# Optimization experiments

Measured on AMD Instinct MI355X. Metric: run time of the kernel, lower is better.

## Reference

```python
import jax, jax.numpy as jnp
import numpy as np

EPS = 1e-5


def conv1x1(x, w):
    # x: (N, C, V, T), w: (O, C) -> (N, O, V, T)
    return jnp.einsum('ncvt,oc->novt', x, w)


def batchnorm2d(y, gamma, beta):
    # training-mode BN over (N, V, T) per channel, biased variance (torch semantics)
    mean = jnp.mean(y, axis=(0, 2, 3), keepdims=True)
    var = jnp.mean((y - mean) ** 2, axis=(0, 2, 3), keepdims=True)
    yhat = (y - mean) * jax.lax.rsqrt(var + EPS)
    return yhat * gamma[None, :, None, None] + beta[None, :, None, None]


def spatial_g(x, wg1, wg2):
    # learned adjacency: softmax over last dim of (N, T, V, V)
    a1 = conv1x1(x, wg1)  # (N, O, V, T)
    a2 = conv1x1(x, wg2)  # (N, O, V, T)
    g = jnp.einsum('novt,nout->ntvu', a1, a2)  # (N, T, V, V)
    return jax.nn.softmax(g, axis=-1)


def gcn_unit(x, g, w1, w2, gamma, beta):
    # message passing: g (N,T,V,V) applied over joint dim of x (N,C,V,T)
    x1 = jnp.einsum('ntvu,ncut->ncvt', g, x)
    y = conv1x1(x1, w1) + conv1x1(x, w2)
    return jax.nn.relu(batchnorm2d(y, gamma, beta))


def setup_inputs() -> dict:
    key = jax.random.key(0)
    ks = jax.random.split(key, 12)
    N, C, V, T = 64, 64, 25, 128
    dims = [64, 64, 128, 256]
    gp = 16
    s = 0.05
    inp = {
        'x': jax.random.normal(ks[0], (N, C, V, T), jnp.float32),
        'wg1': jax.random.normal(ks[1], (gp, dims[0]), jnp.float32) * s,
        'wg2': jax.random.normal(ks[2], (gp, dims[0]), jnp.float32) * s,
        'w11': jax.random.normal(ks[3], (dims[1], dims[0]), jnp.float32) * s,
        'w12': jax.random.normal(ks[4], (dims[1], dims[0]), jnp.float32) * s,
        'gamma1': jnp.ones((dims[1],), jnp.float32),
        'beta1': jnp.zeros((dims[1],), jnp.float32),
        'w21': jax.random.normal(ks[5], (dims[2], dims[1]), jnp.float32) * s,
        'w22': jax.random.normal(ks[6], (dims[2], dims[1]), jnp.float32) * s,
        'gamma2': jnp.ones((dims[2],), jnp.float32),
        'beta2': jnp.zeros((dims[2],), jnp.float32),
        'w31': jax.random.normal(ks[7], (dims[3], dims[2]), jnp.float32) * s,
        'w32': jax.random.normal(ks[8], (dims[3], dims[2]), jnp.float32) * s,
        'gamma3': jnp.ones((dims[3],), jnp.float32),
        'beta3': jnp.zeros((dims[3],), jnp.float32),
    }
    return inp


def reference(x, wg1, wg2, w11, w12, gamma1, beta1, w21, w22, gamma2, beta2,
              w31, w32, gamma3, beta3):
    g = spatial_g(x, wg1, wg2)                       # shared adjacency (N,T,V,V)
    x = gcn_unit(x, g, w11, w12, gamma1, beta1)      # (N, 64, V, T)
    x = gcn_unit(x, g, w21, w22, gamma2, beta2)      # (N, 128, V, T)
    x = gcn_unit(x, g, w31, w32, gamma3, beta3)      # (N, 256, V, T)
    return x, g
```

## Files before the change

kernel.cpp:

```cpp
#include <hip/hip_runtime.h>
#include <cstdint>

#define V_ 25
#define T_ 128
#define VT_ 3200
#define NVTF_ 204800.0f

typedef unsigned short ushort_t;
typedef __attribute__((ext_vector_type(8))) short s16x8;
typedef __attribute__((ext_vector_type(4))) float f32x4;

__device__ __forceinline__ ushort_t f2bf(float f) {
    union { float f; unsigned u; } v; v.f = f;
    unsigned r = v.u + 0x7FFFu + ((v.u >> 16) & 1u);
    return (ushort_t)(r >> 16);
}
__device__ __forceinline__ float bf2f(ushort_t h) {
    union { unsigned u; float f; } v; v.u = ((unsigned)h) << 16;
    return v.f;
}
__device__ __forceinline__ void gload16(const void* g, void* l) {
    __builtin_amdgcn_global_load_lds((const __attribute__((address_space(1))) void*)g,
                                     (__attribute__((address_space(3))) void*)l, 16, 0, 0);
}

__global__ __launch_bounds__(128) void k_a(const float* __restrict__ x,
        const float* __restrict__ wg1, const float* __restrict__ wg2,
        ushort_t* __restrict__ a1, ushort_t* __restrict__ a2,
        ushort_t* __restrict__ xb) {
    int b = blockIdx.x; int n = b / V_; int v = b % V_;
    int t = threadIdx.x;
    __shared__ float w1s[1024], w2s[1024];
    for (int i = threadIdx.x; i < 1024; i += 128) { w1s[i] = wg1[i]; w2s[i] = wg2[i]; }
    __syncthreads();
    float s1[16], s2[16];
    #pragma unroll
    for (int o = 0; o < 16; o++) { s1[o] = 0.f; s2[o] = 0.f; }
    s16x8 xs[8];
    const float* xp = x + (size_t)n * 204800 + v * T_ + t;
    #pragma unroll
    for (int c = 0; c < 64; c++) {
        float xv = xp[(size_t)c * VT_];
        xs[c >> 3][c & 7] = (short)f2bf(xv);
        #pragma unroll
        for (int o = 0; o < 16; o++) {
            s1[o] = fmaf(w1s[o*64+c], xv, s1[o]);
            s2[o] = fmaf(w2s[o*64+c], xv, s2[o]);
        }
    }
    size_t abase = (size_t)n * 51200 + v * T_ + t;
    #pragma unroll
    for (int o = 0; o < 16; o++) {
        a1[abase + (size_t)o * VT_] = f2bf(s1[o]);
        a2[abase + (size_t)o * VT_] = f2bf(s2[o]);
    }
    ushort_t* cp = xb + (size_t)(n * VT_ + v * T_ + t) * 64;
    #pragma unroll
    for (int ch = 0; ch < 8; ch++) *(s16x8*)(cp + ch * 8) = xs[ch];
}

__global__ __launch_bounds__(256) void k_g(const ushort_t* __restrict__ a1,
        const ushort_t* __restrict__ a2, float* __restrict__ g,
        ushort_t* __restrict__ gb) {
    int n = blockIdx.x >> 3; int t0 = (blockIdx.x & 7) * 16;
    __shared__ float A1s[6400], A2s[6400];
    for (int i = threadIdx.x; i < 6400; i += 256) {
        int o = i / 400; int r = i % 400; int v = r >> 4; int tt = r & 15;
        size_t ga = (size_t)n * 51200 + (size_t)o * VT_ + v * T_ + t0 + tt;
        A1s[i] = bf2f(a1[ga]);
        A2s[i] = bf2f(a2[ga]);
    }
    __syncthreads();
    for (int r = threadIdx.x; r < 400; r += 256) {
        int v = r >> 4; int tt = r & 15;
        float a1r[16];
        #pragma unroll
        for (int o = 0; o < 16; o++) a1r[o] = A1s[o*400 + v*16 + tt];
        float gr[25];
        float mx = -1e30f;
        for (int u = 0; u < 25; u++) {
            float s = 0.f;
            #pragma unroll
            for (int o = 0; o < 16; o++) s = fmaf(a1r[o], A2s[o*400 + u*16 + tt], s);
            gr[u] = s; mx = fmaxf(mx, s);
        }
        float sum = 0.f;
        for (int u = 0; u < 25; u++) { gr[u] = __expf(gr[u] - mx); sum += gr[u]; }
        float inv = 1.f / sum;
        float* gp = g + ((size_t)(n * T_ + t0 + tt) * V_ + v) * V_;
        ushort_t* gbp = gb + ((size_t)((n * 128 + t0 + tt) * 25 + v)) * 32;
        for (int u = 0; u < 25; u++) {
            float val = gr[u] * inv;
            gp[u] = val;
            gbp[u] = f2bf(val);
        }
    }
}

__global__ void k_wcat(const float* __restrict__ w11, const float* __restrict__ w12,
        const float* __restrict__ w21, const float* __restrict__ w22,
        const float* __restrict__ w31, const float* __restrict__ w32,
        ushort_t* __restrict__ Wc) {
    int i = blockIdx.x * 256 + threadIdx.x;
    float v;
    if (i < 8192) {
        int o = i >> 7, k = i & 127;
        v = (k < 64) ? w11[o * 64 + k] : w12[o * 64 + k - 64];
    } else if (i < 24576) {
        int j = i - 8192; int o = j >> 7, k = j & 127;
        v = (k < 64) ? w21[o * 64 + k] : w22[o * 64 + k - 64];
    } else {
        int j = i - 24576; int o = j >> 8, k = j & 255;
        v = (k < 128) ? w31[o * 128 + k] : w32[o * 128 + k - 128];
    }
    Wc[i] = f2bf(v);
}

template<int C, bool BNB, bool XBSRC, int TOUT, int OPASS>
__global__ __launch_bounds__(256) void k_fgemm(
        const ushort_t* __restrict__ Wc, const ushort_t* __restrict__ ysrc,
        const ushort_t* __restrict__ gb,
        const float* __restrict__ bns, const float* __restrict__ bnb,
        ushort_t* __restrict__ yt,
        float* __restrict__ psum, float* __restrict__ psq) {
    constexpr int K2 = 2 * C;
    constexpr int KSTEPS = K2 / 32;
    constexpr int NC8 = C / 8;
    constexpr int HKS = C / 32;
    constexpr int MROWS = 100;
    constexpr int MI = 7;
    constexpr int CW = (C == 64) ? 1 : 2;
    constexpr int XBYTES = (TOUT == 0) ? 14400 : 11200;
    __shared__ __align__(16) ushort_t YS[MROWS * C];
    __shared__ __align__(16) ushort_t MPo[MROWS * C];
    __shared__ __align__(16) char XTRA[XBYTES];
    float* GS = (float*)XTRA;
    ushort_t* Lw = (ushort_t*)XTRA;

    int n = blockIdx.y, mb = blockIdx.x;
    int m0 = mb * MROWS, tb = mb * 4;
    int tid = threadIdx.x, w = tid >> 6, lane = tid & 63;
    int l15 = lane & 15, g4 = lane >> 4;

    for (int i = tid; i < 2500; i += 256) {
        int tl = i / 625, r = i % 625, u = r / 25, v = r % 25;
        GS[(tl * 25 + u) * 28 + v] =
            bf2f(gb[((size_t)((n * 128 + tb + tl) * 25 + v)) * 32 + u]);
    }
    for (int i = tid; i < MROWS * NC8; i += 256) {
        int yr = i / NC8, cc = i % NC8;
        size_t saddr;
        if (XBSRC) {
            int t = tb + yr / 25, v = yr % 25;
            saddr = (size_t)n * 204800 + (size_t)(v * 128 + t) * 64 + cc * 8;
        } else {
            saddr = ((size_t)n * VT_ + m0 + yr) * C + cc * 8;
        }
        s16x8 vv = *(const s16x8*)(ysrc + saddr);
        if (BNB) {
            int ob = cc * 8;
            float4 s0 = *(const float4*)(bns + ob), s1 = *(const float4*)(bns + ob + 4);
            float4 h0 = *(const float4*)(bnb + ob), h1 = *(const float4*)(bnb + ob + 4);
            float sc[8] = {s0.x, s0.y, s0.z, s0.w, s1.x, s1.y, s1.z, s1.w};
            float sh[8] = {h0.x, h0.y, h0.z, h0.w, h1.x, h1.y, h1.z, h1.w};
            #pragma unroll
            for (int j = 0; j < 8; j++) {
                float f = fmaf(bf2f((ushort_t)vv[j]), sc[j], sh[j]);
                vv[j] = (short)f2bf(fmaxf(f, 0.f));
            }
        }
        *(s16x8*)(YS + ((size_t)yr * NC8 + (cc ^ (yr & 7))) * 8) = vv;
    }
    __syncthreads();
    {
        int cwi = tid & 63;
        int tl = tid >> 6;
        int c8 = (cwi * CW) >> 3;
        int sub = (cwi * CW) & 7;
        float macc[25][CW];
        #pragma unroll
        for (int v = 0; v < 25; v++)
            #pragma unroll
            for (int k = 0; k < CW; k++) macc[v][k] = 0.f;
        for (int u = 0; u < 25; u++) {
            int yr = tl * 25 + u;
            const ushort_t* yp = YS + ((size_t)yr * NC8 + (c8 ^ (yr & 7))) * 8 + sub;
            float yf[CW];
            if (CW == 2) {
                unsigned yw = *(const unsigned*)yp;
                yf[0] = bf2f((ushort_t)(yw & 0xFFFFu));
                yf[1] = bf2f((ushort_t)(yw >> 16));
            } else {
                yf[0] = bf2f(*yp);
            }
            const float* gp = &GS[(tl * 25 + u) * 28];
            float gv[25];
            #pragma unroll
            for (int q = 0; q < 6; q++) {
                float4 gq = *(const float4*)(gp + q * 4);
                gv[q*4+0] = gq.x; gv[q*4+1] = gq.y; gv[q*4+2] = gq.z; gv[q*4+3] = gq.w;
            }
            gv[24] = gp[24];
            #pragma unroll
            for (int v = 0; v < 25; v++)
                #pragma unroll
                for (int k = 0; k < CW; k++)
                    macc[v][k] = fmaf(gv[v], yf[k], macc[v][k]);
        }
        #pragma unroll
        for (int v = 0; v < 25; v++) {
            int r = tl * 25 + v;
            ushort_t* op = MPo + ((size_t)r * NC8 + (c8 ^ (r & 7))) * 8 + sub;
            if (CW == 2) {
                unsigned w2 = (unsigned)f2bf(macc[v][0]) | ((unsigned)f2bf(macc[v][1]) << 16);
                *(unsigned*)op = w2;
            } else {
                *op = f2bf(macc[v][0]);
            }
        }
    }
    __syncthreads();
    for (int pass = 0; pass < OPASS; pass++) {
        int o0 = pass * 64;
        s16x8 aReg[KSTEPS];
        const ushort_t* ap = Wc + (size_t)(o0 + w * 16 + l15) * K2 + g4 * 8;
        #pragma unroll
        for (int ks = 0; ks < KSTEPS; ks++)
            aReg[ks] = *(const s16x8*)(ap + ks * 32);
        f32x4 acc[MI] = {};
        __builtin_amdgcn_s_setprio(1);
        #pragma unroll
        for (int ks = 0; ks < KSTEPS; ks++) {
            const ushort_t* bbase = (ks < HKS) ? MPo : YS;
            int ksl = (ks < HKS) ? ks : ks - HKS;
            #pragma unroll
            for (int mi = 0; mi < MI; mi++) {
                int r = mi * 16 + l15;
                int rr = (r < MROWS) ? r : (MROWS - 1);
                int ch = ksl * 4 + g4;
                s16x8 bF = *(const s16x8*)(bbase + ((size_t)rr * NC8 + (ch ^ (rr & 7))) * 8);
                acc[mi] = __builtin_amdgcn_mfma_f32_16x16x32_bf16(aReg[ks], bF, acc[mi], 0, 0, 0);
            }
        }
        __builtin_amdgcn_s_setprio(0);
        int p = n * 32 + mb;
        #pragma unroll
        for (int b = 0; b < 4; b++) {
            float ss = 0.f, qq = 0.f;
            #pragma unroll
            for (int mi = 0; mi < MI; mi++) {
                float v0 = acc[mi][b];
                if (mi == 6 && l15 >= 4) v0 = 0.f;
                ss += v0; qq = fmaf(v0, v0, qq);
            }
            #pragma unroll
            for (int msk = 1; msk < 16; msk <<= 1) {
                ss += __shfl_xor(ss, msk, 16);
                qq += __shfl_xor(qq, msk, 16);
            }
            if (l15 == 0) {
                int o = o0 + w * 16 + g4 * 4 + b;
                psum[(size_t)o * 2048 + p] = ss;
                psq [(size_t)o * 2048 + p] = qq;
            }
        }
        if (TOUT == 0) {
            __syncthreads();
            #pragma unroll
            for (int mi = 0; mi < MI; mi++) {
                int r = mi * 16 + l15;
                if (r < MROWS) {
                    #pragma unroll
                    for (int b = 0; b < 4; b++)
                        Lw[r * 72 + w * 16 + g4 * 4 + b] = f2bf(acc[mi][b]);
                }
            }
            __syncthreads();
            for (int i = tid; i < MROWS * 8; i += 256) {
                int r = i >> 3, oc = i & 7;
                s16x8 pk = *(const s16x8*)(Lw + r * 72 + oc * 8);
                *(s16x8*)(yt + ((size_t)n * VT_ + m0 + r) * (OPASS * 64) + o0 + oc * 8) = pk;
            }
        } else {
            int obase = n * 256 + o0 + w * 16 + g4 * 4;
            #pragma unroll
            for (int mi = 0; mi < MI; mi++) {
                int r = mi * 16 + l15;
                if (r < MROWS) {
                    #pragma unroll
                    for (int b = 0; b < 4; b++)
                        yt[(size_t)(obase + b) * VT_ + m0 + r] = f2bf(acc[mi][b]);
                }
            }
        }
    }
}

__global__ __launch_bounds__(256) void k_stats(const float* __restrict__ psum,
        const float* __restrict__ psq, const float* __restrict__ gamma,
        const float* __restrict__ beta, float* __restrict__ bns,
        float* __restrict__ bnb) {
    int o = blockIdx.x;
    float s = 0.f, q = 0.f;
    for (int i = threadIdx.x; i < 2048; i += 256) {
        s += psum[(size_t)o*2048+i]; q += psq[(size_t)o*2048+i];
    }
    __shared__ float rs[256], rq[256];
    rs[threadIdx.x] = s; rq[threadIdx.x] = q;
    __syncthreads();
    for (int st = 128; st > 0; st >>= 1) {
        if (threadIdx.x < st) { rs[threadIdx.x] += rs[threadIdx.x+st]; rq[threadIdx.x] += rq[threadIdx.x+st]; }
        __syncthreads();
    }
    if (threadIdx.x == 0) {
        float mean = rs[0] / NVTF_;
        float var = rq[0] / NVTF_ - mean * mean;
        float scale = gamma[o] * rsqrtf(var + 1e-5f);
        bns[o] = scale;
        bnb[o] = beta[o] - mean * scale;
    }
}

__global__ __launch_bounds__(256) void k_bnf(const ushort_t* __restrict__ y3,
        const float* __restrict__ bns, const float* __restrict__ bnb,
        float* __restrict__ xout) {
    __shared__ __align__(16) ushort_t L[8 * VT_];
    int n = blockIdx.y, oc = blockIdx.x;
    size_t base = (size_t)(n * 256 + oc * 8) * VT_;
    for (int i = threadIdx.x; i < 3200; i += 256)
        gload16(y3 + base + (size_t)i * 8, (char*)L + i * 16);
    __syncthreads();
    for (int i = threadIdx.x; i < 6400; i += 256) {
        int t4 = i & 31, v = (i >> 5) % 25, o = i / 800;
        int og = oc * 8 + o;
        float sc = bns[og], sh = bnb[og];
        int lb = o * VT_ + v;
        float4 f;
        f.x = fmaxf(fmaf(bf2f(L[lb + (t4*4+0)*25]), sc, sh), 0.f);
        f.y = fmaxf(fmaf(bf2f(L[lb + (t4*4+1)*25]), sc, sh), 0.f);
        f.z = fmaxf(fmaf(bf2f(L[lb + (t4*4+2)*25]), sc, sh), 0.f);
        f.w = fmaxf(fmaf(bf2f(L[lb + (t4*4+3)*25]), sc, sh), 0.f);
        *(float4*)(xout + (size_t)(n * 256 + og) * VT_ + v * T_ + t4 * 4) = f;
    }
}

extern "C" void kernel_launch(void* const* d_in, const int* in_sizes, int n_in,
                              void* d_out, int out_size, void* d_ws, size_t ws_size,
                              hipStream_t stream) {
    const float* x   = (const float*)d_in[0];
    const float* wg1 = (const float*)d_in[1];
    const float* wg2 = (const float*)d_in[2];
    const float* w11 = (const float*)d_in[3];
    const float* w12 = (const float*)d_in[4];
    const float* ga1 = (const float*)d_in[5];
    const float* be1 = (const float*)d_in[6];
    const float* w21 = (const float*)d_in[7];
    const float* w22 = (const float*)d_in[8];
    const float* ga2 = (const float*)d_in[9];
    const float* be2 = (const float*)d_in[10];
    const float* w31 = (const float*)d_in[11];
    const float* w32 = (const float*)d_in[12];
    const float* ga3 = (const float*)d_in[13];
    const float* be3 = (const float*)d_in[14];

    float* xout = (float*)d_out;
    float* gout = xout + 52428800;

    float* ws = (float*)d_ws;
    ushort_t* xb  = (ushort_t*)(ws + 0);
    ushort_t* a1  = (ushort_t*)(ws + 6553600);
    ushort_t* a2  = (ushort_t*)(ws + 8192000);
    ushort_t* y1  = (ushort_t*)(ws + 9830400);
    ushort_t* y2  = (ushort_t*)(ws + 16384000);
    ushort_t* y3  = (ushort_t*)(ws + 29491200);
    ushort_t* gb  = (ushort_t*)(ws + 55705600);
    float* psum = ws + 58982400;
    float* psq  = ws + 59506688;
    ushort_t* Wc = (ushort_t*)(ws + 60030976);
    float* bns  = ws + 60076032;
    float* bnb  = ws + 60076288;
    ushort_t* Wc1 = Wc, *Wc2 = Wc + 8192, *Wc3 = Wc + 24576;

    k_a<<<1600, 128, 0, stream>>>(x, wg1, wg2, a1, a2, xb);
    k_g<<<512, 256, 0, stream>>>(a1, a2, gout, gb);
    k_wcat<<<352, 256, 0, stream>>>(w11, w12, w21, w22, w31, w32, Wc);

    k_fgemm<64, false, true, 0, 1><<<dim3(32, 64), 256, 0, stream>>>(
        Wc1, xb, gb, nullptr, nullptr, y1, psum, psq);
    k_stats<<<64, 256, 0, stream>>>(psum, psq, ga1, be1, bns, bnb);

    k_fgemm<64, true, false, 0, 2><<<dim3(32, 64), 256, 0, stream>>>(
        Wc2, y1, gb, bns, bnb, y2, psum, psq);
    k_stats<<<128, 256, 0, stream>>>(psum, psq, ga2, be2, bns, bnb);

    k_fgemm<128, true, false, 2, 4><<<dim3(32, 64), 256, 0, stream>>>(
        Wc3, y2, gb, bns, bnb, y3, psum, psq);
    k_stats<<<256, 256, 0, stream>>>(psum, psq, ga3, be3, bns, bnb);

    k_bnf<<<dim3(32, 64), 256, 0, stream>>>(y3, bns, bnb, xout);
}
```

Before: 341.1 us.

## Halve fused GEMM tile to two timesteps, fold weight concat into k_a

```diff
diff --git a/kernel.cpp b/kernel.cpp
--- a/kernel.cpp
+++ b/kernel.cpp
@@ -19,6 +19,11 @@
     union { unsigned u; float f; } v; v.u = ((unsigned)h) << 16;
     return v.f;
 }
+__device__ __forceinline__ unsigned cvtpk(float lo, float hi) {
+    unsigned r;
+    asm volatile("v_cvt_pk_bf16_f32 %0, %1, %2" : "=v"(r) : "v"(lo), "v"(hi));
+    return r;
+}
 __device__ __forceinline__ void gload16(const void* g, void* l) {
     __builtin_amdgcn_global_load_lds((const __attribute__((address_space(1))) void*)g,
                                      (__attribute__((address_space(3))) void*)l, 16, 0, 0);
@@ -27,9 +32,28 @@
 __global__ __launch_bounds__(128) void k_a(const float* __restrict__ x,
         const float* __restrict__ wg1, const float* __restrict__ wg2,
         ushort_t* __restrict__ a1, ushort_t* __restrict__ a2,
-        ushort_t* __restrict__ xb) {
+        ushort_t* __restrict__ xb,
+        const float* __restrict__ w11, const float* __restrict__ w12,
+        const float* __restrict__ w21, const float* __restrict__ w22,
+        const float* __restrict__ w31, const float* __restrict__ w32,
+        ushort_t* __restrict__ Wc) {
     int b = blockIdx.x; int n = b / V_; int v = b % V_;
     int t = threadIdx.x;
+    int wi = b * 128 + t;
+    if (wi < 90112) {
+        float wv;
+        if (wi < 8192) {
+            int o = wi >> 7, k = wi & 127;
+            wv = (k < 64) ? w11[o * 64 + k] : w12[o * 64 + k - 64];
+        } else if (wi < 24576) {
+            int j = wi - 8192; int o = j >> 7, k = j & 127;
+            wv = (k < 64) ? w21[o * 64 + k] : w22[o * 64 + k - 64];
+        } else {
+            int j = wi - 24576; int o = j >> 8, k = j & 255;
+            wv = (k < 128) ? w31[o * 128 + k] : w32[o * 128 + k - 128];
+        }
+        Wc[wi] = f2bf(wv);
+    }
     __shared__ float w1s[1024], w2s[1024];
     for (int i = threadIdx.x; i < 1024; i += 128) { w1s[i] = wg1[i]; w2s[i] = wg2[i]; }
     __syncthreads();
@@ -95,25 +119,6 @@
             gbp[u] = f2bf(val);
         }
     }
-}
-
-__global__ void k_wcat(const float* __restrict__ w11, const float* __restrict__ w12,
-        const float* __restrict__ w21, const float* __restrict__ w22,
-        const float* __restrict__ w31, const float* __restrict__ w32,
-        ushort_t* __restrict__ Wc) {
-    int i = blockIdx.x * 256 + threadIdx.x;
-    float v;
-    if (i < 8192) {
-        int o = i >> 7, k = i & 127;
-        v = (k < 64) ? w11[o * 64 + k] : w12[o * 64 + k - 64];
-    } else if (i < 24576) {
-        int j = i - 8192; int o = j >> 7, k = j & 127;
-        v = (k < 64) ? w21[o * 64 + k] : w22[o * 64 + k - 64];
-    } else {
-        int j = i - 24576; int o = j >> 8, k = j & 255;
-        v = (k < 128) ? w31[o * 128 + k] : w32[o * 128 + k - 128];
-    }
-    Wc[i] = f2bf(v);
 }
 
 template<int C, bool BNB, bool XBSRC, int TOUT, int OPASS>
@@ -127,10 +132,12 @@
     constexpr int KSTEPS = K2 / 32;
     constexpr int NC8 = C / 8;
     constexpr int HKS = C / 32;
-    constexpr int MROWS = 100;
-    constexpr int MI = 7;
-    constexpr int CW = (C == 64) ? 1 : 2;
-    constexpr int XBYTES = (TOUT == 0) ? 14400 : 11200;
+    constexpr int TG = 2;
+    constexpr int MROWS = 50;
+    constexpr int MI = 4;
+    constexpr int VSPLIT = 128 / C;
+    constexpr int GSB = TG * 25 * 28 * 4;
+    constexpr int XBYTES = (TOUT == 0) ? (MROWS * 72 * 2) : GSB;
     __shared__ __align__(16) ushort_t YS[MROWS * C];
     __shared__ __align__(16) ushort_t MPo[MROWS * C];
     __shared__ __align__(16) char XTRA[XBYTES];
@@ -138,11 +145,11 @@
     ushort_t* Lw = (ushort_t*)XTRA;
 
     int n = blockIdx.y, mb = blockIdx.x;
-    int m0 = mb * MROWS, tb = mb * 4;
+    int m0 = mb * MROWS, tb = mb * TG;
     int tid = threadIdx.x, w = tid >> 6, lane = tid & 63;
     int l15 = lane & 15, g4 = lane >> 4;
 
-    for (int i = tid; i < 2500; i += 256) {
+    for (int i = tid; i < TG * 625; i += 256) {
         int tl = i / 625, r = i % 625, u = r / 25, v = r % 25;
         GS[(tl * 25 + u) * 28 + v] =
             bf2f(gb[((size_t)((n * 128 + tb + tl) * 25 + v)) * 32 + u]);
@@ -163,59 +170,61 @@
             float4 h0 = *(const float4*)(bnb + ob), h1 = *(const float4*)(bnb + ob + 4);
             float sc[8] = {s0.x, s0.y, s0.z, s0.w, s1.x, s1.y, s1.z, s1.w};
             float sh[8] = {h0.x, h0.y, h0.z, h0.w, h1.x, h1.y, h1.z, h1.w};
-            #pragma unroll
-            for (int j = 0; j < 8; j++) {
-                float f = fmaf(bf2f((ushort_t)vv[j]), sc[j], sh[j]);
-                vv[j] = (short)f2bf(fmaxf(f, 0.f));
-            }
+            float ff[8];
+            #pragma unroll
+            for (int j = 0; j < 8; j++)
+                ff[j] = fmaxf(fmaf(bf2f((ushort_t)vv[j]), sc[j], sh[j]), 0.f);
+            union { unsigned u[4]; s16x8 s; } U;
+            U.u[0] = cvtpk(ff[0], ff[1]); U.u[1] = cvtpk(ff[2], ff[3]);
+            U.u[2] = cvtpk(ff[4], ff[5]); U.u[3] = cvtpk(ff[6], ff[7]);
+            vv = U.s;
         }
         *(s16x8*)(YS + ((size_t)yr * NC8 + (cc ^ (yr & 7))) * 8) = vv;
     }
     __syncthreads();
     {
-        int cwi = tid & 63;
-        int tl = tid >> 6;
-        int c8 = (cwi * CW) >> 3;
-        int sub = (cwi * CW) & 7;
-        float macc[25][CW];
-        #pragma unroll
-        for (int v = 0; v < 25; v++)
-            #pragma unroll
-            for (int k = 0; k < CW; k++) macc[v][k] = 0.f;
+        int tl = tid >> 7;
+        int rem = tid & 127;
+        int col = rem % C;
+        int hv = (VSPLIT == 2) ? (rem / C) : 0;
+        int c8 = col >> 3, sub = col & 7;
+        constexpr int VN = (VSPLIT == 2) ? 13 : 25;
+        int v0 = hv * 12;
+        int vcnt = (VSPLIT == 2) ? (hv ? 13 : 12) : 25;
+        float macc[VN];
+        #pragma unroll
+        for (int j = 0; j < VN; j++) macc[j] = 0.f;
         for (int u = 0; u < 25; u++) {
             int yr = tl * 25 + u;
-            const ushort_t* yp = YS + ((size_t)yr * NC8 + (c8 ^ (yr & 7))) * 8 + sub;
-            float yf[CW];
-            if (CW == 2) {
-                unsigned yw = *(const unsigned*)yp;
-                yf[0] = bf2f((ushort_t)(yw & 0xFFFFu));
-                yf[1] = bf2f((ushort_t)(yw >> 16));
+            float yf = bf2f(YS[((size_t)yr * NC8 + (c8 ^ (yr & 7))) * 8 + sub]);
+            const float* gp = &GS[(tl * 25 + u) * 28] + v0;
+            if (VSPLIT == 1) {
+                #pragma unroll
+                for (int q = 0; q < 6; q++) {
+                    float4 gq = *(const float4*)(gp + q * 4);
+                    macc[q*4+0] = fmaf(gq.x, yf, macc[q*4+0]);
+                    macc[q*4+1] = fmaf(gq.y, yf, macc[q*4+1]);
+                    macc[q*4+2] = fmaf(gq.z, yf, macc[q*4+2]);
+                    macc[q*4+3] = fmaf(gq.w, yf, macc[q*4+3]);
+                }
+                macc[24] = fmaf(gp[24], yf, macc[24]);
             } else {
-                yf[0] = bf2f(*yp);
-            }
-            const float* gp = &GS[(tl * 25 + u) * 28];
-            float gv[25];
-            #pragma unroll
-            for (int q = 0; q < 6; q++) {
-                float4 gq = *(const float4*)(gp + q * 4);
-                gv[q*4+0] = gq.x; gv[q*4+1] = gq.y; gv[q*4+2] = gq.z; gv[q*4+3] = gq.w;
-            }
-            gv[24] = gp[24];
-            #pragma unroll
-            for (int v = 0; v < 25; v++)
                 #pragma unroll
-                for (int k = 0; k < CW; k++)
-                    macc[v][k] = fmaf(gv[v], yf[k], macc[v][k]);
-        }
-        #pragma unroll
-        for (int v = 0; v < 25; v++) {
-            int r = tl * 25 + v;
-            ushort_t* op = MPo + ((size_t)r * NC8 + (c8 ^ (r & 7))) * 8 + sub;
-            if (CW == 2) {
-                unsigned w2 = (unsigned)f2bf(macc[v][0]) | ((unsigned)f2bf(macc[v][1]) << 16);
-                *(unsigned*)op = w2;
-            } else {
-                *op = f2bf(macc[v][0]);
+                for (int q = 0; q < 3; q++) {
+                    float4 gq = *(const float4*)(gp + q * 4);
+                    macc[q*4+0] = fmaf(gq.x, yf, macc[q*4+0]);
+                    macc[q*4+1] = fmaf(gq.y, yf, macc[q*4+1]);
+                    macc[q*4+2] = fmaf(gq.z, yf, macc[q*4+2]);
+                    macc[q*4+3] = fmaf(gq.w, yf, macc[q*4+3]);
+                }
+                if (hv) macc[12] = fmaf(gp[12], yf, macc[12]);
+            }
+        }
+        #pragma unroll
+        for (int j = 0; j < VN; j++) {
+            if (j < vcnt) {
+                int r = tl * 25 + v0 + j;
+                MPo[((size_t)r * NC8 + (c8 ^ (r & 7))) * 8 + sub] = f2bf(macc[j]);
             }
         }
     }
@@ -243,14 +252,14 @@
             }
         }
         __builtin_amdgcn_s_setprio(0);
-        int p = n * 32 + mb;
+        int p = n * 64 + mb;
         #pragma unroll
         for (int b = 0; b < 4; b++) {
             float ss = 0.f, qq = 0.f;
             #pragma unroll
             for (int mi = 0; mi < MI; mi++) {
                 float v0 = acc[mi][b];
-                if (mi == 6 && l15 >= 4) v0 = 0.f;
+                if (mi == 3 && l15 >= 2) v0 = 0.f;
                 ss += v0; qq = fmaf(v0, v0, qq);
             }
             #pragma unroll
@@ -260,8 +269,8 @@
             }
             if (l15 == 0) {
                 int o = o0 + w * 16 + g4 * 4 + b;
-                psum[(size_t)o * 2048 + p] = ss;
-                psq [(size_t)o * 2048 + p] = qq;
+                psum[(size_t)o * 4096 + p] = ss;
+                psq [(size_t)o * 4096 + p] = qq;
             }
         }
         if (TOUT == 0) {
@@ -270,9 +279,10 @@
             for (int mi = 0; mi < MI; mi++) {
                 int r = mi * 16 + l15;
                 if (r < MROWS) {
-                    #pragma unroll
-                    for (int b = 0; b < 4; b++)
-                        Lw[r * 72 + w * 16 + g4 * 4 + b] = f2bf(acc[mi][b]);
+                    unsigned lo = cvtpk(acc[mi][0], acc[mi][1]);
+                    unsigned hi = cvtpk(acc[mi][2], acc[mi][3]);
+                    *(unsigned*)(Lw + r * 72 + w * 16 + g4 * 4)     = lo;
+                    *(unsigned*)(Lw + r * 72 + w * 16 + g4 * 4 + 2) = hi;
                 }
             }
             __syncthreads();
@@ -302,8 +312,8 @@
         float* __restrict__ bnb) {
     int o = blockIdx.x;
     float s = 0.f, q = 0.f;
-    for (int i = threadIdx.x; i < 2048; i += 256) {
-        s += psum[(size_t)o*2048+i]; q += psq[(size_t)o*2048+i];
+    for (int i = threadIdx.x; i < 4096; i += 256) {
+        s += psum[(size_t)o*4096+i]; q += psq[(size_t)o*4096+i];
     }
     __shared__ float rs[256], rq[256];
     rs[threadIdx.x] = s; rq[threadIdx.x] = q;
@@ -375,25 +385,25 @@
     ushort_t* y3  = (ushort_t*)(ws + 29491200);
     ushort_t* gb  = (ushort_t*)(ws + 55705600);
     float* psum = ws + 58982400;
-    float* psq  = ws + 59506688;
-    ushort_t* Wc = (ushort_t*)(ws + 60030976);
-    float* bns  = ws + 60076032;
-    float* bnb  = ws + 60076288;
+    float* psq  = ws + 60030976;
+    ushort_t* Wc = (ushort_t*)(ws + 61079552);
+    float* bns  = ws + 61124608;
+    float* bnb  = ws + 61124864;
     ushort_t* Wc1 = Wc, *Wc2 = Wc + 8192, *Wc3 = Wc + 24576;
 
-    k_a<<<1600, 128, 0, stream>>>(x, wg1, wg2, a1, a2, xb);
+    k_a<<<1600, 128, 0, stream>>>(x, wg1, wg2, a1, a2, xb,
+                                  w11, w12, w21, w22, w31, w32, Wc);
     k_g<<<512, 256, 0, stream>>>(a1, a2, gout, gb);
-    k_wcat<<<352, 256, 0, stream>>>(w11, w12, w21, w22, w31, w32, Wc);
-
-    k_fgemm<64, false, true, 0, 1><<<dim3(32, 64), 256, 0, stream>>>(
+
+    k_fgemm<64, false, true, 0, 1><<<dim3(64, 64), 256, 0, stream>>>(
         Wc1, xb, gb, nullptr, nullptr, y1, psum, psq);
     k_stats<<<64, 256, 0, stream>>>(psum, psq, ga1, be1, bns, bnb);
 
-    k_fgemm<64, true, false, 0, 2><<<dim3(32, 64), 256, 0, stream>>>(
+    k_fgemm<64, true, false, 0, 2><<<dim3(64, 64), 256, 0, stream>>>(
         Wc2, y1, gb, bns, bnb, y2, psum, psq);
     k_stats<<<128, 256, 0, stream>>>(psum, psq, ga2, be2, bns, bnb);
 
-    k_fgemm<128, true, false, 2, 4><<<dim3(32, 64), 256, 0, stream>>>(
+    k_fgemm<128, true, false, 2, 4><<<dim3(64, 64), 256, 0, stream>>>(
         Wc3, y2, gb, bns, bnb, y3, psum, psq);
     k_stats<<<256, 256, 0, stream>>>(psum, psq, ga3, be3, bns, bnb);
 
```

Result: slower. 361.0 us (+5.8%).
